# Kernel tuning notes

Hardware: AMD Instinct MI355X
Metric: run time of the kernel (lower is better)

Reference implementation:

```python
import jax, jax.numpy as jnp
import numpy as np

EPS = 1e-15
BALL_EPS = 4e-3   # geoopt float32 projection eps
N_DST = 20000
N_EDGE = 200000
DIM = 128
H, D = 2, 128


def _norm(x):
    return jnp.sqrt(jnp.maximum(jnp.sum(x * x, -1, keepdims=True), EPS * EPS))


def _artanh(x):
    return jnp.arctanh(jnp.clip(x, -1.0 + 1e-7, 1.0 - 1e-7))


def mobius_add(x, y):
    x2 = jnp.sum(x * x, -1, keepdims=True)
    y2 = jnp.sum(y * y, -1, keepdims=True)
    xy = jnp.sum(x * y, -1, keepdims=True)
    num = (1 + 2 * xy + y2) * x + (1 - x2) * y
    den = 1 + 2 * xy + x2 * y2
    return num / jnp.maximum(den, EPS)


def mobius_matvec(W, x):
    xn = _norm(x)
    mx = x @ W.T
    mxn = _norm(mx)
    return jnp.tanh(mxn / xn * _artanh(xn)) * mx / mxn


def logmap0(y):
    yn = _norm(y)
    return _artanh(yn) * y / yn


def expmap0(u):
    un = _norm(u)
    return jnp.tanh(un) * u / un


def projx(x):
    n = _norm(x)
    maxn = 1.0 - BALL_EPS
    return jnp.where(n > maxn, x * (maxn / n), x)


def ball_dist(x, y):
    # dist(x,y) = 2 artanh(|| (-x) (+) y ||)
    return 2.0 * _artanh(_norm(mobius_add(-x, y))[..., 0])


def edge_softmax(logits, dst, n_dst):
    # softmax over edges grouped by destination node, per trailing dims
    m = jax.ops.segment_max(logits, dst, num_segments=n_dst)
    z = jnp.exp(logits - m[dst])
    s = jax.ops.segment_sum(z, dst, num_segments=n_dst)
    return z / s[dst]


def setup_inputs() -> dict:
    key = jax.random.key(0)
    ks = jax.random.split(key, 8)
    hyper = expmap0(0.2 * jax.random.normal(ks[0], (N_DST + N_EDGE, DIM), jnp.float32))
    dt = jax.random.uniform(ks[1], (N_EDGE,), jnp.float32) * 1e4
    time_w = jnp.asarray(1.0 / 10 ** np.linspace(0, 9, DIM, dtype=np.float32))
    time_b = jnp.zeros((DIM,), jnp.float32)
    w_src = 0.05 * jax.random.normal(ks[2], (H * D, DIM), jnp.float32)
    b_src = 0.01 * jax.random.normal(ks[3], (H * D,), jnp.float32)
    w_dst = 0.05 * jax.random.normal(ks[4], (H * D, DIM), jnp.float32)
    b_dst = 0.01 * jax.random.normal(ks[5], (H * D,), jnp.float32)
    attn = 0.1 * jax.random.normal(ks[6], (1, H, D), jnp.float32)
    src_idx = jnp.arange(N_EDGE, dtype=jnp.int32) + N_DST  # edge i's src node
    dst_idx = jax.random.randint(ks[7], (N_EDGE,), 0, N_DST, jnp.int32)
    return {"hyper": hyper, "dt": dt, "time_w": time_w, "time_b": time_b,
            "w_src": w_src, "b_src": b_src, "w_dst": w_dst, "b_dst": b_dst,
            "attn": attn, "src_idx": src_idx, "dst_idx": dst_idx}


def reference(hyper, dt, time_w, time_b, w_src, b_src, w_dst, b_dst, attn, src_idx, dst_idx):
    n_dst = N_DST
    # time encoding: zeros for dst nodes, dt for the sampled neighbor of each edge
    time = jnp.concatenate([jnp.zeros((n_dst,), dt.dtype), dt])        # [num_src]
    time_feat = jnp.cos(time[:, None] * time_w[None, :] + time_b)      # [num_src, DIM]
    time_feat = projx(time_feat)
    src_feat = mobius_add(hyper, time_feat)                            # [num_src, DIM]
    h_dst = src_feat[:n_dst]
    feat_src = mobius_add(mobius_matvec(w_src, src_feat), b_src)       # [num_src, H*D]
    feat_dst = mobius_add(mobius_matvec(w_dst, h_dst), b_dst)          # [n_dst, H*D]
    el = logmap0(feat_src).reshape(-1, H, D)
    er = logmap0(feat_dst).reshape(-1, H, D)
    # attention logit per edge/head
    e = jnp.sum((el[src_idx] + er[dst_idx]) * attn, -1)[:, :, None]    # [E,H,1]
    # hyperbolic-distance gate, edge-softmax normalized
    d = ball_dist(feat_src[src_idx], feat_dst[dst_idx])                # [E]
    inv = 1.0 / (1e-15 + d)
    dsm = edge_softmax(inv[:, None], dst_idx, n_dst)[:, :, None]       # [E,1,1]
    e = jax.nn.leaky_relu(e * dsm, 0.2)
    a = edge_softmax(e, dst_idx, n_dst)                                # [E,H,1]
    ft = jax.ops.segment_sum(el[src_idx] * a, dst_idx, num_segments=n_dst)
    rst = ft.reshape(n_dst, H * D)
    return expmap0(rst)
```

## Files before the change

kernel.cpp:

```cpp
#include <hip/hip_runtime.h>
#include <hip/hip_bf16.h>
#include <math.h>

typedef __attribute__((ext_vector_type(8))) short bfrag8;
typedef __attribute__((ext_vector_type(4))) float ffrag4;

__device__ inline float bf2f(unsigned short h) { return __uint_as_float(((unsigned)h) << 16); }
__device__ inline unsigned short f2bf(float f) {
    unsigned u = __float_as_uint(f);
    unsigned r = (u + 0x7FFFu + ((u >> 16) & 1u)) >> 16;
    return (unsigned short)r;
}
__device__ inline float wred(float v) {
    v += __shfl_xor(v, 1, 64);
    v += __shfl_xor(v, 2, 64);
    v += __shfl_xor(v, 4, 64);
    v += __shfl_xor(v, 8, 64);
    v += __shfl_xor(v, 16, 64);
    v += __shfl_xor(v, 32, 64);
    return v;
}
__device__ inline float wredmax(float v) {
    v = fmaxf(v, __shfl_xor(v, 1, 64));
    v = fmaxf(v, __shfl_xor(v, 2, 64));
    v = fmaxf(v, __shfl_xor(v, 4, 64));
    v = fmaxf(v, __shfl_xor(v, 8, 64));
    v = fmaxf(v, __shfl_xor(v, 16, 64));
    v = fmaxf(v, __shfl_xor(v, 32, 64));
    return v;
}
__device__ inline float bsum(float v, float* red) {
    v = wred(v);
    if ((threadIdx.x & 63) == 0) red[threadIdx.x >> 6] = v;
    __syncthreads();
    float r = red[0] + red[1] + red[2] + red[3];
    __syncthreads();
    return r;
}

#define ACLIP (1.0f - 1e-7f)
#define ATANH_ACLIP 8.4056196f

__device__ inline float rcpf(float x) { return __builtin_amdgcn_rcpf(x); }
__device__ inline float fsqrtf(float x) { return __builtin_amdgcn_sqrtf(x); }
__device__ inline float fexp(float x) { return __expf(x); }
__device__ inline float flog(float x) { return __logf(x); }
__device__ inline float atanh_over_x(float x) {
    if (x < 0.125f) {
        float x2 = x * x;
        return 1.0f + x2 * (0.33333333f + x2 * 0.2f);
    }
    return 0.5f * flog((1.0f + x) * rcpf(1.0f - x)) * rcpf(x);
}
__device__ inline float tanh_over_x(float x) {
    if (x < 0.125f) {
        float x2 = x * x;
        return 1.0f - x2 * (0.33333333f - x2 * 0.13333333f);
    }
    float e = fexp(-2.0f * x);
    return (1.0f - e) * rcpf((1.0f + e) * x);
}
__device__ inline float fcosr(float x) {
    const float C  = 0.15915494309189535f;
    const float C1 = 0.1591796875f;
    const float C2 = -2.4744408e-5f;
    float k = __builtin_rintf(x * C);
    float f = fmaf(x, C1, -k);
    f = fmaf(x, C2, f);
    return __builtin_amdgcn_cosf(f);
}

__global__ void k_detect(const unsigned short* __restrict__ hyper, int* __restrict__ flag) {
    __shared__ int total;
    int t = threadIdx.x;
    if (t == 0) total = 0;
    __syncthreads();
    int cnt = 0;
    for (int i = t * 8; i < t * 8 + 8; i++) {
        if ((i & 1) == 0) {
            unsigned e = ((unsigned)hyper[i] >> 7) & 0xFF;
            if (e >= 0xC0) cnt++;
        }
    }
    atomicAdd(&total, cnt);
    __syncthreads();
    if (t == 0) *flag = (total >= 32) ? 1 : 0;
}

__device__ inline float ldin(const void* s, int i, int isf32) {
    return isf32 ? ((const float*)s)[i] : bf2f(((const unsigned short*)s)[i]);
}
__global__ void k_params(const void* __restrict__ w_src, const void* __restrict__ w_dst,
                         const void* __restrict__ b_src, const void* __restrict__ b_dst,
                         const void* __restrict__ attn, const void* __restrict__ time_w,
                         const void* __restrict__ time_b,
                         unsigned short* __restrict__ whs, unsigned short* __restrict__ wls,
                         unsigned short* __restrict__ whd, unsigned short* __restrict__ wld,
                         float* __restrict__ bsrc, float* __restrict__ bdst,
                         float* __restrict__ pattn, float* __restrict__ tw,
                         float* __restrict__ tb, const int* __restrict__ flag, int nw) {
    int i = blockIdx.x * blockDim.x + threadIdx.x;
    int isf32 = *flag;
    if (i < nw) {
        float x = ldin(w_src, i, isf32);
        unsigned short h = f2bf(x);
        whs[i] = h; wls[i] = f2bf(x - bf2f(h));
        float y = ldin(w_dst, i, isf32);
        unsigned short g = f2bf(y);
        whd[i] = g; wld[i] = f2bf(y - bf2f(g));
    }
    if (i < 256) {
        bsrc[i] = ldin(b_src, i, isf32);
        bdst[i] = ldin(b_dst, i, isf32);
        pattn[i] = ldin(attn, i, isf32);
    }
    if (i < 128) {
        tw[i] = ldin(time_w, i, isf32);
        tb[i] = ldin(time_b, i, isf32);
    }
}
__global__ void k_fill(unsigned* __restrict__ p, unsigned v, int n) {
    int i = blockIdx.x * blockDim.x + threadIdx.x;
    if (i < n) p[i] = v;
}

__global__ void k_hist(const int* __restrict__ dst_idx, int* __restrict__ deg, int n_edge) {
    int i = blockIdx.x * blockDim.x + threadIdx.x;
    if (i < n_edge) atomicAdd(deg + dst_idx[i], 1);
}
__global__ __launch_bounds__(1024) void k_scan(const int* __restrict__ deg,
                                               int* __restrict__ rowptr,
                                               int* __restrict__ cursor, int n) {
    __shared__ int part[1024];
    int t = threadIdx.x;
    int chunk = (n + 1023) >> 10;
    int lo = t * chunk, hi = min(lo + chunk, n);
    int s = 0;
    for (int i = lo; i < hi; i++) s += deg[i];
    part[t] = s;
    __syncthreads();
    for (int dd = 1; dd < 1024; dd <<= 1) {
        int v = (t >= dd) ? part[t - dd] : 0;
        __syncthreads();
        part[t] += v;
        __syncthreads();
    }
    int base = (t == 0) ? 0 : part[t - 1];
    for (int i = lo; i < hi; i++) {
        rowptr[i] = base; cursor[i] = base;
        base += deg[i];
    }
    if (t == 0) rowptr[n] = part[1023];
}
__global__ void k_scatter_edges(const int* __restrict__ src_idx, const int* __restrict__ dst_idx,
                                int* __restrict__ cursor, int* __restrict__ es, int n_edge) {
    int i = blockIdx.x * blockDim.x + threadIdx.x;
    if (i >= n_edge) return;
    int slot = atomicAdd(cursor + dst_idx[i], 1);
    es[slot] = src_idx[i];
}

__global__ void k_node_prep(const void* __restrict__ hyper_v,
                            const void* __restrict__ dt_v,
                            const float* __restrict__ tw, const float* __restrict__ tb,
                            unsigned short* __restrict__ Ah, unsigned short* __restrict__ Al,
                            float* __restrict__ tnode,
                            const int* __restrict__ flag, int n_dst, int n_total) {
    int wid  = (blockIdx.x * blockDim.x + threadIdx.x) >> 6;
    int lane = threadIdx.x & 63;
    if (wid >= n_total) return;
    int isf32 = *flag;
    float tval = 0.0f;
    if (wid >= n_dst) {
        int e = wid - n_dst;
        tval = isf32 ? ((const float*)dt_v)[e] : bf2f(((const unsigned short*)dt_v)[e]);
    }
    int j0 = lane * 2;
    float tf0 = fcosr(tval * tw[j0]     + tb[j0]);
    float tf1 = fcosr(tval * tw[j0 + 1] + tb[j0 + 1]);
    float h0, h1;
    if (isf32) {
        const float* hp = (const float*)hyper_v + (size_t)wid * 128 + j0;
        h0 = hp[0]; h1 = hp[1];
    } else {
        const unsigned short* hp = (const unsigned short*)hyper_v + (size_t)wid * 128 + j0;
        h0 = bf2f(hp[0]); h1 = bf2f(hp[1]);
    }
    float ptf2 = wred(tf0 * tf0 + tf1 * tf1);
    float ph2  = wred(h0 * h0 + h1 * h1);
    float pht  = wred(h0 * tf0 + h1 * tf1);
    float ntf = fsqrtf(fmaxf(ptf2, 1e-30f));
    float maxn = 1.0f - 0.004f;
    float sc = (ntf > maxn) ? (maxn * rcpf(ntf)) : 1.0f;
    float y2 = sc * sc * ptf2, xy = sc * pht, x2 = ph2;
    float A = 1.0f + 2.0f * xy + y2;
    float B = 1.0f - x2;
    float iden = rcpf(fmaxf(1.0f + 2.0f * xy + x2 * y2, 1e-15f));
    float s0 = (A * h0 + B * sc * tf0) * iden;
    float s1 = (A * h1 + B * sc * tf1) * iden;
    unsigned short h0s = f2bf(s0), h1s = f2bf(s1);
    unsigned short l0s = f2bf(s0 - bf2f(h0s)), l1s = f2bf(s1 - bf2f(h1s));
    *(ushort2*)(Ah + (size_t)wid * 128 + j0) = make_ushort2(h0s, h1s);
    *(ushort2*)(Al + (size_t)wid * 128 + j0) = make_ushort2(l0s, l1s);
    float ps2 = wred(s0 * s0 + s1 * s1);
    float xn = fsqrtf(fmaxf(ps2, 1e-30f));
    float g = (xn > ACLIP) ? (ATANH_ACLIP * rcpf(xn)) : atanh_over_x(xn);
    if (lane == 0) tnode[wid] = g;
}

#define WPITCH 72
#define GEMM_LDS (256 * WPITCH * 2 * 2)
__global__ __launch_bounds__(512, 4) void k_gemm_ep(
        const unsigned short* __restrict__ Ah, const unsigned short* __restrict__ Al,
        const unsigned short* __restrict__ Wh, const unsigned short* __restrict__ Wl,
        const float* __restrict__ bvec, const float* __restrict__ attn,
        const float* __restrict__ tnode,
        float* __restrict__ feat, float* __restrict__ x2a, float* __restrict__ ca,
        float* __restrict__ satt, int base, int M) {
    extern __shared__ unsigned short smem[];
    unsigned short* Bhs = smem;
    unsigned short* Bls = smem + 256 * WPITCH;

    int t = threadIdx.x;
    auto stage = [&](int hf) {
        for (int v = t; v < 2048; v += 512) {
            int e = v << 3;
            int row = e >> 6, col = e & 63;
            *(bfrag8*)(Bhs + row * WPITCH + col) = *(const bfrag8*)(Wh + row * 128 + hf * 64 + col);
            *(bfrag8*)(Bls + row * WPITCH + col) = *(const bfrag8*)(Wl + row * 128 + hf * 64 + col);
        }
    };

    int w = t >> 6, lane = t & 63;
    int m16 = lane & 15, kg = lane >> 4;
    int rowbase = (blockIdx.x * 8 + w) * 16;
    int ar0 = min(rowbase + m16, M - 1);
    const unsigned short* A0h = Ah + (size_t)ar0 * 128;
    const unsigned short* A0l = Al + (size_t)ar0 * 128;

    ffrag4 acc[16];
#pragma unroll
    for (int ct = 0; ct < 16; ct++) acc[ct] = (ffrag4){0.0f, 0.0f, 0.0f, 0.0f};

    stage(0);
    int kA = kg * 8;
    bfrag8 ah0 = *(const bfrag8*)(A0h + 0 * 32 + kA);
    bfrag8 al0 = *(const bfrag8*)(A0l + 0 * 32 + kA);
    bfrag8 ah1 = *(const bfrag8*)(A0h + 1 * 32 + kA);
    bfrag8 al1 = *(const bfrag8*)(A0l + 1 * 32 + kA);
    bfrag8 ah2 = *(const bfrag8*)(A0h + 2 * 32 + kA);
    bfrag8 al2 = *(const bfrag8*)(A0l + 2 * 32 + kA);
    bfrag8 ah3 = *(const bfrag8*)(A0h + 3 * 32 + kA);
    bfrag8 al3 = *(const bfrag8*)(A0l + 3 * 32 + kA);
    __syncthreads();

    auto kstep = [&](bfrag8 ahk, bfrag8 alk, int kc) {
#pragma unroll
        for (int ct = 0; ct < 16; ct++) {
            int wb = (ct * 16 + m16) * WPITCH + kc;
            bfrag8 bh = *(const bfrag8*)(Bhs + wb);
            bfrag8 bl = *(const bfrag8*)(Bls + wb);
            acc[ct] = __builtin_amdgcn_mfma_f32_16x16x32_bf16(ahk, bh, acc[ct], 0, 0, 0);
            acc[ct] = __builtin_amdgcn_mfma_f32_16x16x32_bf16(alk, bh, acc[ct], 0, 0, 0);
            acc[ct] = __builtin_amdgcn_mfma_f32_16x16x32_bf16(ahk, bl, acc[ct], 0, 0, 0);
        }
    };

    kstep(ah0, al0, kA);
    kstep(ah1, al1, 32 + kA);
    __syncthreads();
    stage(1);
    __syncthreads();
    kstep(ah2, al2, kA);
    kstep(ah3, al3, 32 + kA);

    float bv[16], av[16];
    float pb2 = 0.0f;
#pragma unroll
    for (int ct = 0; ct < 16; ct++) {
        bv[ct] = bvec[ct * 16 + m16];
        av[ct] = attn[ct * 16 + m16];
        pb2 += bv[ct] * bv[ct];
    }
#pragma unroll
    for (int off = 1; off < 16; off <<= 1) pb2 += __shfl_xor(pb2, off, 64);

    float pm2[4] = {0, 0, 0, 0}, pdb[4] = {0, 0, 0, 0};
#pragma unroll
    for (int ct = 0; ct < 16; ct++)
#pragma unroll
        for (int r = 0; r < 4; r++) {
            float v = acc[ct][r];
            pm2[r] += v * v;
            pdb[r] += v * bv[ct];
        }
#pragma unroll
    for (int off = 1; off < 16; off <<= 1)
#pragma unroll
        for (int r = 0; r < 4; r++) {
            pm2[r] += __shfl_xor(pm2[r], off, 64);
            pdb[r] += __shfl_xor(pdb[r], off, 64);
        }
#pragma unroll
    for (int r = 0; r < 4; r++) {
        int row_o = rowbase + kg * 4 + r;
        bool ok = row_o < M;
        float g = ok ? tnode[base + row_o] : 1.0f;
        float mxn = fsqrtf(fmaxf(pm2[r], 1e-30f));
        float sv = g * tanh_over_x(mxn * g);
        float xy = sv * pdb[r];
        float x2v = sv * sv * pm2[r];
        float Am = 1.0f + 2.0f * xy + pb2;
        float Bm = 1.0f - x2v;
        float iden = rcpf(fmaxf(1.0f + 2.0f * xy + x2v * pb2, 1e-15f));
        float pf2 = 0.0f, pa0 = 0.0f, pa1 = 0.0f;
#pragma unroll
        for (int ct = 0; ct < 16; ct++) {
            float f = (Am * sv * acc[ct][r] + Bm * bv[ct]) * iden;
            acc[ct][r] = f;
            pf2 += f * f;
            if (ct < 8) pa0 += f * av[ct]; else pa1 += f * av[ct];
        }
#pragma unroll
        for (int off = 1; off < 16; off <<= 1) {
            pf2 += __shfl_xor(pf2, off, 64);
            pa0 += __shfl_xor(pa0, off, 64);
            pa1 += __shfl_xor(pa1, off, 64);
        }
        if (ok) {
            float* fr = feat + (size_t)(base + row_o) * 256;
#pragma unroll
            for (int ct = 0; ct < 16; ct++) fr[ct * 16 + m16] = acc[ct][r];
            if (m16 == 0) {
                float nf = fsqrtf(fmaxf(pf2, 1e-30f));
                float cl = (nf > ACLIP) ? (ATANH_ACLIP * rcpf(nf)) : atanh_over_x(nf);
                x2a[base + row_o] = pf2;
                ca[base + row_o] = cl;
                satt[(size_t)(base + row_o) * 2 + 0] = cl * pa0;
                satt[(size_t)(base + row_o) * 2 + 1] = cl * pa1;
            }
        }
    }
}

#define CAPR 16
#define CAPE 64
__global__ __launch_bounds__(256) void k_aggregate(
        const int* __restrict__ rowptr, const int* __restrict__ es,
        const float* __restrict__ x2a, const float* __restrict__ satt,
        const float* __restrict__ ca, const float* __restrict__ feat,
        float* __restrict__ invg, float* __restrict__ w0g, float* __restrict__ w1g,
        void* __restrict__ out, const int* __restrict__ flag, int n_dst) {
    __shared__ float red[4];
    __shared__ float yrow[256];
    __shared__ float inv_s[CAPE], w0_s[CAPE], w1_s[CAPE];
    __shared__ int sb_s[CAPE];
    __shared__ float cache[CAPR * 256];
    int d = blockIdx.x;
    int t = threadIdx.x;
    int w = t >> 6, lane = t & 63;
    int off0 = rowptr[d], off1 = rowptr[d + 1];
    int deg = off1 - off0;
    if (deg == 0) {
        if (*flag) ((float*)out)[(size_t)d * 256 + t] = 0.0f;
        else ((unsigned short*)out)[(size_t)d * 256 + t] = 0;
        return;
    }
    yrow[t] = feat[(size_t)d * 256 + t];
    float y2 = x2a[d];
    __syncthreads();

    int g16 = lane >> 4, sub = lane & 15;
    int cb = sub * 16;
    float4 yv0 = *(const float4*)(&yrow[cb + 0]);
    float4 yv1 = *(const float4*)(&yrow[cb + 4]);
    float4 yv2 = *(const float4*)(&yrow[cb + 8]);
    float4 yv3 = *(const float4*)(&yrow[cb + 12]);
    for (int b = 0; b < deg; b += 16) {
        int j = b + w * 4 + g16;
        if (j < deg) {
            int i = off0 + j;
            int s = es[i];
            const float* xr = feat + (size_t)s * 256 + cb;
            float4 x0 = *(const float4*)(xr + 0);
            float4 x1 = *(const float4*)(xr + 4);
            float4 x2f = *(const float4*)(xr + 8);
            float4 x3 = *(const float4*)(xr + 12);
            float pd = x0.x * yv0.x + x0.y * yv0.y + x0.z * yv0.z + x0.w * yv0.w
                     + x1.x * yv1.x + x1.y * yv1.y + x1.z * yv1.z + x1.w * yv1.w
                     + x2f.x * yv2.x + x2f.y * yv2.y + x2f.z * yv2.z + x2f.w * yv2.w
                     + x3.x * yv3.x + x3.y * yv3.y + x3.z * yv3.z + x3.w * yv3.w;
            pd += __shfl_xor(pd, 1, 64);
            pd += __shfl_xor(pd, 2, 64);
            pd += __shfl_xor(pd, 4, 64);
            pd += __shfl_xor(pd, 8, 64);
            if (j < CAPR) {
                float* cr = &cache[j * 256 + cb];
                *(float4*)(cr + 0) = x0;
                *(float4*)(cr + 4) = x1;
                *(float4*)(cr + 8) = x2f;
                *(float4*)(cr + 12) = x3;
            }
            if (sub == 0) {
                float x2 = x2a[s];
                float A = 1.0f - 2.0f * pd + y2;
                float B = 1.0f - x2;
                float iden = rcpf(fmaxf(1.0f - 2.0f * pd + x2 * y2, 1e-15f));
                float p2 = fmaxf(A * A * x2 - 2.0f * A * B * pd + B * B * y2, 0.0f);
                float nrm = fsqrtf(fmaxf(p2, 1e-30f)) * iden;
                float xc = fminf(nrm, ACLIP);
                float dd = 2.0f * xc * atanh_over_x(xc);
                float iv = rcpf(1e-15f + dd);
                if (j < CAPE) { inv_s[j] = iv; sb_s[j] = s; }
                else { invg[i] = iv; }
            }
        }
    }
    __syncthreads();

    if (w == 0) {
        float sd0 = satt[(size_t)d * 2 + 0], sd1 = satt[(size_t)d * 2 + 1];
        if (deg <= CAPE) {
            int j = lane;
            bool act = j < deg;
            int s = act ? sb_s[j] : 0;
            float iv = act ? inv_s[j] : -INFINITY;
            float m1 = wredmax(iv);
            float z = fexp(iv - m1);
            float is1 = rcpf(wred(z));
            float dsm = z * is1;
            float a0 = act ? satt[(size_t)s * 2 + 0] : 0.0f;
            float a1 = act ? satt[(size_t)s * 2 + 1] : 0.0f;
            float e0 = (a0 + sd0) * dsm; e0 = (e0 > 0.0f) ? e0 : 0.2f * e0;
            float e1 = (a1 + sd1) * dsm; e1 = (e1 > 0.0f) ? e1 : 0.2f * e1;
            float m20 = wredmax(act ? e0 : -INFINITY);
            float m21 = wredmax(act ? e1 : -INFINITY);
            float z0 = act ? fexp(e0 - m20) : 0.0f;
            float z1 = act ? fexp(e1 - m21) : 0.0f;
            float is20 = rcpf(wred(z0));
            float is21 = rcpf(wred(z1));
            if (act) {
                float cs = ca[s];
                w0_s[j] = z0 * is20 * cs;
                w1_s[j] = z1 * is21 * cs;
            }
        } else {
            float lm = -INFINITY;
            for (int j = lane; j < deg; j += 64)
                lm = fmaxf(lm, (j < CAPE) ? inv_s[j] : invg[off0 + j]);
            float m1 = wredmax(lm);
            float ls = 0.0f;
            for (int j = lane; j < deg; j += 64)
                ls += fexp(((j < CAPE) ? inv_s[j] : invg[off0 + j]) - m1);
            float is1 = rcpf(wred(ls));
            float lm0 = -INFINITY, lm1 = -INFINITY;
            for (int j = lane; j < deg; j += 64) {
                int s = (j < CAPE) ? sb_s[j] : es[off0 + j];
                float iv = (j < CAPE) ? inv_s[j] : invg[off0 + j];
                float dsm = fexp(iv - m1) * is1;
                float e0 = (satt[(size_t)s * 2 + 0] + sd0) * dsm; e0 = (e0 > 0.0f) ? e0 : 0.2f * e0;
                float e1 = (satt[(size_t)s * 2 + 1] + sd1) * dsm; e1 = (e1 > 0.0f) ? e1 : 0.2f * e1;
                if (j < CAPE) { w0_s[j] = e0; w1_s[j] = e1; }
                else { w0g[off0 + j] = e0; w1g[off0 + j] = e1; }
                lm0 = fmaxf(lm0, e0); lm1 = fmaxf(lm1, e1);
            }
            float m20 = wredmax(lm0), m21 = wredmax(lm1);
            float l20 = 0.0f, l21 = 0.0f;
            for (int j = lane; j < deg; j += 64) {
                float e0 = (j < CAPE) ? w0_s[j] : w0g[off0 + j];
                float e1 = (j < CAPE) ? w1_s[j] : w1g[off0 + j];
                l20 += fexp(e0 - m20); l21 += fexp(e1 - m21);
            }
            float is20 = rcpf(wred(l20)), is21 = rcpf(wred(l21));
            for (int j = lane; j < deg; j += 64) {
                int s = (j < CAPE) ? sb_s[j] : es[off0 + j];
                float cs = ca[s];
                if (j < CAPE) {
                    w0_s[j] = fexp(w0_s[j] - m20) * is20 * cs;
                    w1_s[j] = fexp(w1_s[j] - m21) * is21 * cs;
                } else {
                    w0g[off0 + j] = fexp(w0g[off0 + j] - m20) * is20 * cs;
                    w1g[off0 + j] = fexp(w1g[off0 + j] - m21) * is21 * cs;
                }
            }
        }
    }
    __syncthreads();

    int col = t, h = t >> 7;
    float acc = 0.0f;
    for (int j = 0; j < deg; j++) {
        float wgt = (j < CAPE) ? (h ? w1_s[j] : w0_s[j])
                               : (h ? w1g[off0 + j] : w0g[off0 + j]);
        float x;
        if (j < CAPR) x = cache[j * 256 + col];
        else {
            int s = (j < CAPE) ? sb_s[j] : es[off0 + j];
            x = feat[(size_t)s * 256 + col];
        }
        acc += wgt * x;
    }
    float p2 = bsum(acc * acc, red);
    float n = fsqrtf(fmaxf(p2, 1e-30f));
    float sc = tanh_over_x(n);
    float o = acc * sc;
    if (*flag) ((float*)out)[(size_t)d * 256 + col] = o;
    else ((unsigned short*)out)[(size_t)d * 256 + col] = f2bf(o);
}

extern "C" void kernel_launch(void* const* d_in, const int* in_sizes, int n_in,
                              void* d_out, int out_size, void* d_ws, size_t ws_size,
                              hipStream_t stream) {
    const void* hyper  = d_in[0];
    const void* dt     = d_in[1];
    const void* time_w = d_in[2];
    const void* time_b = d_in[3];
    const void* w_src  = d_in[4];
    const void* b_src  = d_in[5];
    const void* w_dst  = d_in[6];
    const void* b_dst  = d_in[7];
    const void* attn   = d_in[8];
    const int* src_idx = (const int*)d_in[9];
    const int* dst_idx = (const int*)d_in[10];

    const int DIMN = 128, HD = 256;
    int n_edge  = in_sizes[1];
    int n_total = in_sizes[0] / DIMN;
    int n_dst   = n_total - n_edge;

    float* ws = (float*)d_ws;
    size_t off = 0;
    auto alloc = [&](size_t n) { float* p = ws + off; off += n; return p; };
    float* p_tw    = alloc(DIMN);
    float* p_tb    = alloc(DIMN);
    float* p_bsrc  = alloc(HD);
    float* p_bdst  = alloc(HD);
    float* p_attn  = alloc(HD);
    int*   p_flag  = (int*)alloc(4);
    unsigned short* p_whs = (unsigned short*)alloc((size_t)HD * DIMN / 2);
    unsigned short* p_wls = (unsigned short*)alloc((size_t)HD * DIMN / 2);
    unsigned short* p_whd = (unsigned short*)alloc((size_t)HD * DIMN / 2);
    unsigned short* p_wld = (unsigned short*)alloc((size_t)HD * DIMN / 2);
    unsigned short* p_ah = (unsigned short*)alloc((size_t)n_total * DIMN / 2);
    unsigned short* p_al = (unsigned short*)alloc((size_t)n_total * DIMN / 2);
    int* p_deg    = (int*)alloc(n_dst);
    int* p_rowptr = (int*)alloc(n_dst + 1);
    int* p_cursor = (int*)alloc(n_dst);
    int* p_es     = (int*)alloc(n_edge);
    float* p_inv  = alloc(n_edge);
    float* p_w0   = alloc(n_edge);
    float* p_w1   = alloc(n_edge);
    float* p_feat  = alloc((size_t)n_total * HD);
    float* p_tnode = alloc(n_total);
    float* p_call  = alloc(n_total);
    float* p_x2    = alloc(n_total);
    float* p_satt  = alloc((size_t)n_total * 2);
    (void)ws_size;

    const int TB = 256;
    auto cdiv = [](int a, int b) { return (a + b - 1) / b; };

    static bool lds_cfg = false;
    if (!lds_cfg) {
        hipFuncSetAttribute(reinterpret_cast<const void*>(k_gemm_ep),
                            hipFuncAttributeMaxDynamicSharedMemorySize, GEMM_LDS);
        lds_cfg = true;
    }

    k_detect<<<1, TB, 0, stream>>>((const unsigned short*)hyper, p_flag);

    k_params<<<cdiv(HD * DIMN, TB), TB, 0, stream>>>(
        w_src, w_dst, b_src, b_dst, attn, time_w, time_b,
        p_whs, p_wls, p_whd, p_wld, p_bsrc, p_bdst, p_attn, p_tw, p_tb,
        p_flag, HD * DIMN);

    k_fill<<<cdiv(n_dst, TB), TB, 0, stream>>>((unsigned*)p_deg, 0u, n_dst);
    k_hist<<<cdiv(n_edge, TB), TB, 0, stream>>>(dst_idx, p_deg, n_edge);
    k_scan<<<1, 1024, 0, stream>>>(p_deg, p_rowptr, p_cursor, n_dst);
    k_scatter_edges<<<cdiv(n_edge, TB), TB, 0, stream>>>(src_idx, dst_idx, p_cursor,
                                                         p_es, n_edge);

    k_node_prep<<<cdiv(n_total, 4), TB, 0, stream>>>(hyper, dt, p_tw, p_tb,
                                                     p_ah, p_al, p_tnode, p_flag,
                                                     n_dst, n_total);

    k_gemm_ep<<<cdiv(n_dst, 128), 512, GEMM_LDS, stream>>>(p_ah, p_al, p_whd, p_wld,
                                                           p_bdst, p_attn, p_tnode,
                                                           p_feat, p_x2, p_call, p_satt,
                                                           0, n_dst);
    k_gemm_ep<<<cdiv(n_edge, 128), 512, GEMM_LDS, stream>>>(p_ah + (size_t)n_dst * DIMN,
                                                            p_al + (size_t)n_dst * DIMN,
                                                            p_whs, p_wls,
                                                            p_bsrc, p_attn, p_tnode,
                                                            p_feat, p_x2, p_call, p_satt,
                                                            n_dst, n_edge);

    k_aggregate<<<n_dst, TB, 0, stream>>>(p_rowptr, p_es, p_x2, p_satt, p_call,
                                          p_feat, p_inv, p_w0, p_w1,
                                          d_out, p_flag, n_dst);
}
```

Baseline: 539.8 us.

## Fuse node preprocessing into GEMM prologue, staging split-bf16 A tiles in LDS

Drops the separate node-prep kernel and computes the time encoding, Möbius add, bf16 hi/lo split and artanh gain inside the GEMM kernel. Results go to LDS instead of global Ah/Al/tnode buffers. Bias and attention vectors are also cached in shared memory rather than held in registers. This removes a global write and read-back of the split activations and one kernel launch. In exchange each GEMM block does serial per-row wave reductions before its MFMA work, and LDS is reused between the A tile and the W tiles.

```diff
diff --git a/kernel.cpp b/kernel.cpp
--- a/kernel.cpp
+++ b/kernel.cpp
@@ -160,68 +160,87 @@
     es[slot] = src_idx[i];
 }
 
-__global__ void k_node_prep(const void* __restrict__ hyper_v,
-                            const void* __restrict__ dt_v,
-                            const float* __restrict__ tw, const float* __restrict__ tb,
-                            unsigned short* __restrict__ Ah, unsigned short* __restrict__ Al,
-                            float* __restrict__ tnode,
-                            const int* __restrict__ flag, int n_dst, int n_total) {
-    int wid  = (blockIdx.x * blockDim.x + threadIdx.x) >> 6;
-    int lane = threadIdx.x & 63;
-    if (wid >= n_total) return;
-    int isf32 = *flag;
-    float tval = 0.0f;
-    if (wid >= n_dst) {
-        int e = wid - n_dst;
-        tval = isf32 ? ((const float*)dt_v)[e] : bf2f(((const unsigned short*)dt_v)[e]);
-    }
-    int j0 = lane * 2;
-    float tf0 = fcosr(tval * tw[j0]     + tb[j0]);
-    float tf1 = fcosr(tval * tw[j0 + 1] + tb[j0 + 1]);
-    float h0, h1;
-    if (isf32) {
-        const float* hp = (const float*)hyper_v + (size_t)wid * 128 + j0;
-        h0 = hp[0]; h1 = hp[1];
-    } else {
-        const unsigned short* hp = (const unsigned short*)hyper_v + (size_t)wid * 128 + j0;
-        h0 = bf2f(hp[0]); h1 = bf2f(hp[1]);
-    }
-    float ptf2 = wred(tf0 * tf0 + tf1 * tf1);
-    float ph2  = wred(h0 * h0 + h1 * h1);
-    float pht  = wred(h0 * tf0 + h1 * tf1);
-    float ntf = fsqrtf(fmaxf(ptf2, 1e-30f));
-    float maxn = 1.0f - 0.004f;
-    float sc = (ntf > maxn) ? (maxn * rcpf(ntf)) : 1.0f;
-    float y2 = sc * sc * ptf2, xy = sc * pht, x2 = ph2;
-    float A = 1.0f + 2.0f * xy + y2;
-    float B = 1.0f - x2;
-    float iden = rcpf(fmaxf(1.0f + 2.0f * xy + x2 * y2, 1e-15f));
-    float s0 = (A * h0 + B * sc * tf0) * iden;
-    float s1 = (A * h1 + B * sc * tf1) * iden;
-    unsigned short h0s = f2bf(s0), h1s = f2bf(s1);
-    unsigned short l0s = f2bf(s0 - bf2f(h0s)), l1s = f2bf(s1 - bf2f(h1s));
-    *(ushort2*)(Ah + (size_t)wid * 128 + j0) = make_ushort2(h0s, h1s);
-    *(ushort2*)(Al + (size_t)wid * 128 + j0) = make_ushort2(l0s, l1s);
-    float ps2 = wred(s0 * s0 + s1 * s1);
-    float xn = fsqrtf(fmaxf(ps2, 1e-30f));
-    float g = (xn > ACLIP) ? (ATANH_ACLIP * rcpf(xn)) : atanh_over_x(xn);
-    if (lane == 0) tnode[wid] = g;
-}
-
+#define APITCH 136
 #define WPITCH 72
 #define GEMM_LDS (256 * WPITCH * 2 * 2)
 __global__ __launch_bounds__(512, 4) void k_gemm_ep(
-        const unsigned short* __restrict__ Ah, const unsigned short* __restrict__ Al,
+        const void* __restrict__ hyper_v, const void* __restrict__ dt_v, int use_dt,
+        const float* __restrict__ tw, const float* __restrict__ tb,
         const unsigned short* __restrict__ Wh, const unsigned short* __restrict__ Wl,
         const float* __restrict__ bvec, const float* __restrict__ attn,
-        const float* __restrict__ tnode,
         float* __restrict__ feat, float* __restrict__ x2a, float* __restrict__ ca,
-        float* __restrict__ satt, int base, int M) {
+        float* __restrict__ satt, const int* __restrict__ flag, int base, int M) {
     extern __shared__ unsigned short smem[];
+    __shared__ float tn_s[128];
+    __shared__ float bv_s[256], av_s[256];
+
+    int t = threadIdx.x;
+    int w = t >> 6, lane = t & 63;
+    int isf32 = *flag;
+
+    if (t < 256) { bv_s[t] = bvec[t]; av_s[t] = attn[t]; }
+
+    unsigned short* Ahs = smem;
+    unsigned short* Als = smem + 128 * APITCH;
+    int j0 = lane * 2;
+    float tw0 = tw[j0], tw1 = tw[j0 + 1];
+    float tb0 = tb[j0], tb1 = tb[j0 + 1];
+    int blk0 = blockIdx.x * 128;
+    for (int rr = 0; rr < 16; rr++) {
+        int lr = w * 16 + rr;
+        int gr = min(blk0 + lr, M - 1);
+        float tval = 0.0f;
+        if (use_dt) tval = isf32 ? ((const float*)dt_v)[gr]
+                                 : bf2f(((const unsigned short*)dt_v)[gr]);
+        float tf0 = fcosr(tval * tw0 + tb0);
+        float tf1 = fcosr(tval * tw1 + tb1);
+        float h0, h1;
+        size_t hoff = (size_t)(base + gr) * 128 + j0;
+        if (isf32) {
+            const float* hp = (const float*)hyper_v + hoff;
+            h0 = hp[0]; h1 = hp[1];
+        } else {
+            const unsigned short* hp = (const unsigned short*)hyper_v + hoff;
+            h0 = bf2f(hp[0]); h1 = bf2f(hp[1]);
+        }
+        float ptf2 = wred(tf0 * tf0 + tf1 * tf1);
+        float ph2  = wred(h0 * h0 + h1 * h1);
+        float pht  = wred(h0 * tf0 + h1 * tf1);
+        float ntf = fsqrtf(fmaxf(ptf2, 1e-30f));
+        float maxn = 1.0f - 0.004f;
+        float sc = (ntf > maxn) ? (maxn * rcpf(ntf)) : 1.0f;
+        float y2 = sc * sc * ptf2, xy = sc * pht, x2 = ph2;
+        float A = 1.0f + 2.0f * xy + y2;
+        float B = 1.0f - x2;
+        float iden = rcpf(fmaxf(1.0f + 2.0f * xy + x2 * y2, 1e-15f));
+        float s0 = (A * h0 + B * sc * tf0) * iden;
+        float s1 = (A * h1 + B * sc * tf1) * iden;
+        unsigned short h0s = f2bf(s0), h1s = f2bf(s1);
+        unsigned short l0s = f2bf(s0 - bf2f(h0s)), l1s = f2bf(s1 - bf2f(h1s));
+        *(ushort2*)(Ahs + lr * APITCH + j0) = make_ushort2(h0s, h1s);
+        *(ushort2*)(Als + lr * APITCH + j0) = make_ushort2(l0s, l1s);
+        float ps2 = wred(s0 * s0 + s1 * s1);
+        float xn = fsqrtf(fmaxf(ps2, 1e-30f));
+        float g = (xn > ACLIP) ? (ATANH_ACLIP * rcpf(xn)) : atanh_over_x(xn);
+        if (lane == 0) tn_s[lr] = g;
+    }
+
+    int m16 = lane & 15, kg = lane >> 4;
+    int kA = kg * 8;
+    const unsigned short* Ar  = Ahs + (w * 16 + m16) * APITCH;
+    const unsigned short* Alr = Als + (w * 16 + m16) * APITCH;
+    bfrag8 ah0 = *(const bfrag8*)(Ar  + 0 * 32 + kA);
+    bfrag8 ah1 = *(const bfrag8*)(Ar  + 1 * 32 + kA);
+    bfrag8 ah2 = *(const bfrag8*)(Ar  + 2 * 32 + kA);
+    bfrag8 ah3 = *(const bfrag8*)(Ar  + 3 * 32 + kA);
+    bfrag8 al0 = *(const bfrag8*)(Alr + 0 * 32 + kA);
+    bfrag8 al1 = *(const bfrag8*)(Alr + 1 * 32 + kA);
+    bfrag8 al2 = *(const bfrag8*)(Alr + 2 * 32 + kA);
+    bfrag8 al3 = *(const bfrag8*)(Alr + 3 * 32 + kA);
+    __syncthreads();
+
     unsigned short* Bhs = smem;
     unsigned short* Bls = smem + 256 * WPITCH;
-
-    int t = threadIdx.x;
     auto stage = [&](int hf) {
         for (int v = t; v < 2048; v += 512) {
             int e = v << 3;
@@ -231,28 +250,9 @@
         }
     };
 
-    int w = t >> 6, lane = t & 63;
-    int m16 = lane & 15, kg = lane >> 4;
-    int rowbase = (blockIdx.x * 8 + w) * 16;
-    int ar0 = min(rowbase + m16, M - 1);
-    const unsigned short* A0h = Ah + (size_t)ar0 * 128;
-    const unsigned short* A0l = Al + (size_t)ar0 * 128;
-
     ffrag4 acc[16];
 #pragma unroll
     for (int ct = 0; ct < 16; ct++) acc[ct] = (ffrag4){0.0f, 0.0f, 0.0f, 0.0f};
-
-    stage(0);
-    int kA = kg * 8;
-    bfrag8 ah0 = *(const bfrag8*)(A0h + 0 * 32 + kA);
-    bfrag8 al0 = *(const bfrag8*)(A0l + 0 * 32 + kA);
-    bfrag8 ah1 = *(const bfrag8*)(A0h + 1 * 32 + kA);
-    bfrag8 al1 = *(const bfrag8*)(A0l + 1 * 32 + kA);
-    bfrag8 ah2 = *(const bfrag8*)(A0h + 2 * 32 + kA);
-    bfrag8 al2 = *(const bfrag8*)(A0l + 2 * 32 + kA);
-    bfrag8 ah3 = *(const bfrag8*)(A0h + 3 * 32 + kA);
-    bfrag8 al3 = *(const bfrag8*)(A0l + 3 * 32 + kA);
-    __syncthreads();
 
     auto kstep = [&](bfrag8 ahk, bfrag8 alk, int kc) {
 #pragma unroll
@@ -266,6 +266,8 @@
         }
     };
 
+    stage(0);
+    __syncthreads();
     kstep(ah0, al0, kA);
     kstep(ah1, al1, 32 + kA);
     __syncthreads();
@@ -274,26 +276,23 @@
     kstep(ah2, al2, kA);
     kstep(ah3, al3, 32 + kA);
 
-    float bv[16], av[16];
     float pb2 = 0.0f;
 #pragma unroll
+    for (int ct = 0; ct < 16; ct++) { float b = bv_s[ct * 16 + m16]; pb2 += b * b; }
+#pragma unroll
+    for (int off = 1; off < 16; off <<= 1) pb2 += __shfl_xor(pb2, off, 64);
+
+    float pm2[4] = {0, 0, 0, 0}, pdb[4] = {0, 0, 0, 0};
+#pragma unroll
     for (int ct = 0; ct < 16; ct++) {
-        bv[ct] = bvec[ct * 16 + m16];
-        av[ct] = attn[ct * 16 + m16];
-        pb2 += bv[ct] * bv[ct];
-    }
-#pragma unroll
-    for (int off = 1; off < 16; off <<= 1) pb2 += __shfl_xor(pb2, off, 64);
-
-    float pm2[4] = {0, 0, 0, 0}, pdb[4] = {0, 0, 0, 0};
-#pragma unroll
-    for (int ct = 0; ct < 16; ct++)
+        float b = bv_s[ct * 16 + m16];
 #pragma unroll
         for (int r = 0; r < 4; r++) {
             float v = acc[ct][r];
             pm2[r] += v * v;
-            pdb[r] += v * bv[ct];
-        }
+            pdb[r] += v * b;
+        }
+    }
 #pragma unroll
     for (int off = 1; off < 16; off <<= 1)
 #pragma unroll
@@ -303,9 +302,10 @@
         }
 #pragma unroll
     for (int r = 0; r < 4; r++) {
-        int row_o = rowbase + kg * 4 + r;
+        int lrow = w * 16 + kg * 4 + r;
+        int row_o = blk0 + lrow;
         bool ok = row_o < M;
-        float g = ok ? tnode[base + row_o] : 1.0f;
+        float g = tn_s[lrow];
         float mxn = fsqrtf(fmaxf(pm2[r], 1e-30f));
         float sv = g * tanh_over_x(mxn * g);
         float xy = sv * pdb[r];
@@ -316,10 +316,11 @@
         float pf2 = 0.0f, pa0 = 0.0f, pa1 = 0.0f;
 #pragma unroll
         for (int ct = 0; ct < 16; ct++) {
-            float f = (Am * sv * acc[ct][r] + Bm * bv[ct]) * iden;
+            float f = (Am * sv * acc[ct][r] + Bm * bv_s[ct * 16 + m16]) * iden;
             acc[ct][r] = f;
             pf2 += f * f;
-            if (ct < 8) pa0 += f * av[ct]; else pa1 += f * av[ct];
+            float a = av_s[ct * 16 + m16];
+            if (ct < 8) pa0 += f * a; else pa1 += f * a;
         }
 #pragma unroll
         for (int off = 1; off < 16; off <<= 1) {
@@ -541,8 +542,6 @@
     unsigned short* p_wls = (unsigned short*)alloc((size_t)HD * DIMN / 2);
     unsigned short* p_whd = (unsigned short*)alloc((size_t)HD * DIMN / 2);
     unsigned short* p_wld = (unsigned short*)alloc((size_t)HD * DIMN / 2);
-    unsigned short* p_ah = (unsigned short*)alloc((size_t)n_total * DIMN / 2);
-    unsigned short* p_al = (unsigned short*)alloc((size_t)n_total * DIMN / 2);
     int* p_deg    = (int*)alloc(n_dst);
     int* p_rowptr = (int*)alloc(n_dst + 1);
     int* p_cursor = (int*)alloc(n_dst);
@@ -551,7 +550,6 @@
     float* p_w0   = alloc(n_edge);
     float* p_w1   = alloc(n_edge);
     float* p_feat  = alloc((size_t)n_total * HD);
-    float* p_tnode = alloc(n_total);
     float* p_call  = alloc(n_total);
     float* p_x2    = alloc(n_total);
     float* p_satt  = alloc((size_t)n_total * 2);
@@ -580,20 +578,12 @@
     k_scatter_edges<<<cdiv(n_edge, TB), TB, 0, stream>>>(src_idx, dst_idx, p_cursor,
                                                          p_es, n_edge);
 
-    k_node_prep<<<cdiv(n_total, 4), TB, 0, stream>>>(hyper, dt, p_tw, p_tb,
-                                                     p_ah, p_al, p_tnode, p_flag,
-                                                     n_dst, n_total);
-
-    k_gemm_ep<<<cdiv(n_dst, 128), 512, GEMM_LDS, stream>>>(p_ah, p_al, p_whd, p_wld,
-                                                           p_bdst, p_attn, p_tnode,
-                                                           p_feat, p_x2, p_call, p_satt,
-                                                           0, n_dst);
-    k_gemm_ep<<<cdiv(n_edge, 128), 512, GEMM_LDS, stream>>>(p_ah + (size_t)n_dst * DIMN,
-                                                            p_al + (size_t)n_dst * DIMN,
-                                                            p_whs, p_wls,
-                                                            p_bsrc, p_attn, p_tnode,
-                                                            p_feat, p_x2, p_call, p_satt,
-                                                            n_dst, n_edge);
+    k_gemm_ep<<<cdiv(n_dst, 128), 512, GEMM_LDS, stream>>>(
+        hyper, nullptr, 0, p_tw, p_tb, p_whd, p_wld, p_bdst, p_attn,
+        p_feat, p_x2, p_call, p_satt, p_flag, 0, n_dst);
+    k_gemm_ep<<<cdiv(n_edge, 128), 512, GEMM_LDS, stream>>>(
+        hyper, dt, 1, p_tw, p_tb, p_whs, p_wls, p_bsrc, p_attn,
+        p_feat, p_x2, p_call, p_satt, p_flag, n_dst, n_edge);
 
     k_aggregate<<<n_dst, TB, 0, stream>>>(p_rowptr, p_es, p_x2, p_satt, p_call,
                                           p_feat, p_inv, p_w0, p_w1,
```

Result: faster. 523.4 us (-3.0%).
